# Kernel optimization log

Measured on AMD Instinct MI355X. Metric: run time of the kernel, lower is better.

Reference implementation:

```python
import jax, jax.numpy as jnp
import numpy as np

T, B, H, V = 128, 32, 1024, 32000


def setup_inputs() -> dict:
    key = jax.random.key(0)
    ks = jax.random.split(key, 8)
    scale = 1.0 / np.sqrt(H)
    return {
        "input": jax.random.normal(ks[0], (T, B, H), dtype=jnp.float32),
        "hidden": jnp.zeros((B, H), dtype=jnp.float32),
        "w_ic": jax.random.uniform(ks[1], (H, H), jnp.float32, -scale, scale),
        "w_ix": jax.random.uniform(ks[2], (H, H), jnp.float32, -scale, scale),
        "w_fc": jax.random.uniform(ks[3], (H, H), jnp.float32, -scale, scale),
        "w_fx": jax.random.uniform(ks[4], (H, H), jnp.float32, -scale, scale),
        "b_i": jnp.zeros((H,), dtype=jnp.float32),
        "b_f": jnp.zeros((H,), dtype=jnp.float32),
        "W_out": jax.random.uniform(ks[5], (V, H), jnp.float32, -scale, scale),
        "b_out": jnp.zeros((V,), dtype=jnp.float32),
    }


def reference(input, hidden, w_ic, w_ix, w_fc, w_fx, b_i, b_f, W_out, b_out):
    # Precompute input projections for all timesteps: [T, B, H]
    ix = jnp.einsum("tbh,kh->tbk", input, w_ix)
    fx = jnp.einsum("tbh,kh->tbk", input, w_fx)

    def step(c, xs):
        ix_t, fx_t, x_t = xs
        i_t = jax.nn.sigmoid(c @ w_ic.T + b_i + ix_t)
        f_t = jax.nn.sigmoid(c @ w_fc.T + b_f + fx_t)
        c_new = i_t * x_t + f_t * c  # RAN gated-additive update
        return c_new, c_new

    hidden_final, outputs = jax.lax.scan(step, hidden, (ix, fx, input))
    logits = jnp.einsum("tbh,vh->tbv", outputs, W_out) + b_out
    log_probs = jax.nn.log_softmax(logits, axis=-1)
    return log_probs, hidden_final
```

## Files before the change

### kernel.cpp

```cpp
#include <hip/hip_runtime.h>

typedef __attribute__((ext_vector_type(4))) float f32x4;
typedef __attribute__((ext_vector_type(8))) short bf16x8;

#define T_DIM 128
#define B_DIM 32
#define H_DIM 1024
#define V_DIM 32000
#define MROWS 4096
#define NBLK 64
#define CSTEP 32768
#define WSTRIDE 1028

__device__ __forceinline__ ushort f2bf(float f){
  union { float f; unsigned u; } x; x.f = f;
  unsigned u = x.u;
  unsigned r = (u + 0x7fffu + ((u >> 16) & 1u)) >> 16;
  return (ushort)r;
}
__device__ __forceinline__ float bf2f(ushort h){
  union { unsigned u; float f; } x; x.u = ((unsigned)h) << 16;
  return x.f;
}

__device__ __forceinline__ void async_copy16(void* lds, const void* g){
  __builtin_amdgcn_global_load_lds((const __attribute__((address_space(1))) void*)g,
                                   (__attribute__((address_space(3))) void*)lds, 16, 0, 0);
}

__global__ void cast_bf16_kernel(const float* __restrict__ s, ushort* __restrict__ d, int n4){
  int stride = gridDim.x * blockDim.x;
  for (int i = blockIdx.x*blockDim.x + threadIdx.x; i < n4; i += stride){
    float4 v = ((const float4*)s)[i];
    ushort4 o = make_ushort4(f2bf(v.x), f2bf(v.y), f2bf(v.z), f2bf(v.w));
    ((ushort4*)d)[i] = o;
  }
}

__global__ void cast_split_kernel(const float* __restrict__ s, ushort* __restrict__ dh,
                                  ushort* __restrict__ dl, int n4){
  int stride = gridDim.x * blockDim.x;
  for (int i = blockIdx.x*blockDim.x + threadIdx.x; i < n4; i += stride){
    float4 v = ((const float4*)s)[i];
    ushort4 h = make_ushort4(f2bf(v.x), f2bf(v.y), f2bf(v.z), f2bf(v.w));
    ushort4 l = make_ushort4(f2bf(v.x - bf2f(h.x)), f2bf(v.y - bf2f(h.y)),
                             f2bf(v.z - bf2f(h.z)), f2bf(v.w - bf2f(h.w)));
    ((ushort4*)dh)[i] = h;
    ((ushort4*)dl)[i] = l;
  }
}

__global__ __launch_bounds__(256) void gemm_bt(
    const ushort* __restrict__ A, const ushort* __restrict__ B,
    float* __restrict__ C, const float* __restrict__ bias,
    int N, int K, int NTN, int order, int achunk,
    float* __restrict__ pmax, float* __restrict__ psum)
{
  __shared__ ushort lA[128*32];
  __shared__ ushort lB[128*32];
  __shared__ float pmS[4][64], psS[4][64];
  int tid = threadIdx.x;
  int lane = tid & 63, wid = tid >> 6;
  int bid = blockIdx.x;
  int tm, tn;
  if (order){
    int xcd = bid & 7, id = bid >> 3;
    tn = id >> 2;
    tm = (xcd << 2) | (id & 3);
  } else {
    tm = bid / NTN; tn = bid % NTN;
  }
  int row0 = tm << 7, col0 = tn << 7;

  f32x4 acc[4][4] = {};

  auto stage = [&](const ushort* __restrict__ g, ushort* l, int r0, int k0){
    int c = wid << 1;
    const ushort* s0 = g + (size_t)(r0 + (c<<4) + (lane>>2))*K + k0 + ((lane&3)<<3);
    async_copy16(l + (c<<9), s0);
    async_copy16(l + ((c+1)<<9), s0 + (size_t)16*K);
  };
  auto stageAc = [&](const ushort* __restrict__ g, ushort* l, int r0, int k0){
    int c = wid << 1;
    int cb  = (k0 >> 4) + ((lane & 3) >> 1);
    int sub = (lane & 1) << 3;
    int rA = r0 + (c<<4) + (lane>>2);
    const ushort* sA = g + ((size_t)(rA>>5)<<15) + (cb<<9) + ((rA&31)<<4) + sub;
    async_copy16(l + (c<<9), sA);
    int rB = rA + 16;
    const ushort* sB = g + ((size_t)(rB>>5)<<15) + (cb<<9) + ((rB&31)<<4) + sub;
    async_copy16(l + ((c+1)<<9), sB);
  };

  int nk = K >> 5;
  if (achunk) stageAc(A, lA, row0, 0); else stage(A, lA, row0, 0);
  stage(B, lB, col0, 0);
  int wm = (wid >> 1) << 6, wn = (wid & 1) << 6;
  int kg = (lane >> 4) << 3;
  int ar = lane & 15;

  for (int kt = 0; kt < nk; ++kt){
    __syncthreads();
    bf16x8 af[4], bfr[4];
    #pragma unroll
    for (int mi = 0; mi < 4; ++mi) af[mi]  = *(const bf16x8*)&lA[(wm + mi*16 + ar)*32 + kg];
    #pragma unroll
    for (int ni = 0; ni < 4; ++ni) bfr[ni] = *(const bf16x8*)&lB[(wn + ni*16 + ar)*32 + kg];
    #pragma unroll
    for (int mi = 0; mi < 4; ++mi)
      #pragma unroll
      for (int ni = 0; ni < 4; ++ni)
        acc[mi][ni] = __builtin_amdgcn_mfma_f32_16x16x32_bf16(af[mi], bfr[ni], acc[mi][ni], 0, 0, 0);
    if (kt + 1 < nk){
      __syncthreads();
      if (achunk) stageAc(A, lA, row0, (kt+1) << 5); else stage(A, lA, row0, (kt+1) << 5);
      stage(B, lB, col0, (kt+1) << 5);
    }
  }

  int rr = (lane >> 4) << 2;
  float bb4[4];
  #pragma unroll
  for (int ni = 0; ni < 4; ++ni) bb4[ni] = bias ? bias[col0 + wn + ni*16 + ar] : 0.f;

  #pragma unroll
  for (int mi = 0; mi < 4; ++mi){
    #pragma unroll
    for (int q = 0; q < 4; ++q){
      int r = row0 + wm + mi*16 + rr + q;
      float vals[4];
      #pragma unroll
      for (int ni = 0; ni < 4; ++ni){
        vals[ni] = acc[mi][ni][q] + bb4[ni];
        C[(size_t)r * N + col0 + wn + ni*16 + ar] = vals[ni];
      }
      if (pmax){
        float m = fmaxf(fmaxf(vals[0], vals[1]), fmaxf(vals[2], vals[3]));
        #pragma unroll
        for (int o = 1; o < 16; o <<= 1) m = fmaxf(m, __shfl_xor(m, o));
        float s = expf(vals[0]-m) + expf(vals[1]-m) + expf(vals[2]-m) + expf(vals[3]-m);
        #pragma unroll
        for (int o = 1; o < 16; o <<= 1) s += __shfl_xor(s, o);
        if (ar == 0){ int rl = mi*16 + rr + q; pmS[wid][rl] = m; psS[wid][rl] = s; }
      }
    }
  }
  if (pmax){
    __syncthreads();
    if (tid < 128){
      int rl = tid & 63, half = tid >> 6;
      int w0 = half*2, w1 = w0 + 1;
      float m0 = pmS[w0][rl], m1 = pmS[w1][rl];
      float s0 = psS[w0][rl], s1 = psS[w1][rl];
      float M = fmaxf(m0, m1);
      float S = s0*expf(m0-M) + s1*expf(m1-M);
      int r = row0 + half*64 + rl;
      pmax[(size_t)r*NTN + tn] = M;
      psum[(size_t)r*NTN + tn] = S;
    }
  }
}

__global__ __launch_bounds__(256) void gemm_bt_split(
    const ushort* __restrict__ Ah, const ushort* __restrict__ Al,
    const ushort* __restrict__ Bh, const ushort* __restrict__ Bl,
    float* __restrict__ C, int N, int K, int NTN)
{
  __shared__ ushort lAh[128*32], lAl[128*32], lBh[128*32], lBl[128*32];
  int tid = threadIdx.x;
  int lane = tid & 63, wid = tid >> 6;
  int tm = blockIdx.x / NTN, tn = blockIdx.x % NTN;
  int row0 = tm << 7, col0 = tn << 7;

  f32x4 acc[4][4] = {};

  auto stage = [&](const ushort* __restrict__ g, ushort* l, int r0, int k0){
    int c = wid << 1;
    const ushort* s0 = g + (size_t)(r0 + (c<<4) + (lane>>2))*K + k0 + ((lane&3)<<3);
    async_copy16(l + (c<<9), s0);
    async_copy16(l + ((c+1)<<9), s0 + (size_t)16*K);
  };

  int nk = K >> 5;
  stage(Ah, lAh, row0, 0); stage(Al, lAl, row0, 0);
  stage(Bh, lBh, col0, 0); stage(Bl, lBl, col0, 0);
  int wm = (wid >> 1) << 6, wn = (wid & 1) << 6;
  int kg = (lane >> 4) << 3;
  int ar = lane & 15;

  for (int kt = 0; kt < nk; ++kt){
    __syncthreads();
    bf16x8 afh[4], afl[4], bfh[4], bfl[4];
    #pragma unroll
    for (int mi = 0; mi < 4; ++mi){
      afh[mi] = *(const bf16x8*)&lAh[(wm + mi*16 + ar)*32 + kg];
      afl[mi] = *(const bf16x8*)&lAl[(wm + mi*16 + ar)*32 + kg];
    }
    #pragma unroll
    for (int ni = 0; ni < 4; ++ni){
      bfh[ni] = *(const bf16x8*)&lBh[(wn + ni*16 + ar)*32 + kg];
      bfl[ni] = *(const bf16x8*)&lBl[(wn + ni*16 + ar)*32 + kg];
    }
    #pragma unroll
    for (int mi = 0; mi < 4; ++mi)
      #pragma unroll
      for (int ni = 0; ni < 4; ++ni){
        acc[mi][ni] = __builtin_amdgcn_mfma_f32_16x16x32_bf16(afh[mi], bfh[ni], acc[mi][ni], 0, 0, 0);
        acc[mi][ni] = __builtin_amdgcn_mfma_f32_16x16x32_bf16(afh[mi], bfl[ni], acc[mi][ni], 0, 0, 0);
        acc[mi][ni] = __builtin_amdgcn_mfma_f32_16x16x32_bf16(afl[mi], bfh[ni], acc[mi][ni], 0, 0, 0);
      }
    if (kt + 1 < nk){
      __syncthreads();
      stage(Ah, lAh, row0, (kt+1) << 5); stage(Al, lAl, row0, (kt+1) << 5);
      stage(Bh, lBh, col0, (kt+1) << 5); stage(Bl, lBl, col0, (kt+1) << 5);
    }
  }

  int rr = (lane >> 4) << 2;
  #pragma unroll
  for (int mi = 0; mi < 4; ++mi)
    #pragma unroll
    for (int ni = 0; ni < 4; ++ni){
      int r  = row0 + wm + mi*16 + rr;
      int cc = col0 + wn + ni*16 + ar;
      #pragma unroll
      for (int q = 0; q < 4; ++q)
        C[(size_t)(r + q) * N + cc] = acc[mi][ni][q];
    }
}

__global__ __launch_bounds__(512) void ran_all(
    const ushort* __restrict__ cinit, ushort* __restrict__ cstate,
    const float* __restrict__ hiddenf,
    const ushort* __restrict__ wh, const ushort* __restrict__ wl,
    const float* __restrict__ b_i, const float* __restrict__ b_f,
    const float* __restrict__ ixfx, const float* __restrict__ x_all,
    float* __restrict__ hid_final, unsigned* __restrict__ slots)
{
  __shared__ ushort lWh[32*WSTRIDE];
  __shared__ ushort lWl[32*WSTRIDE];
  __shared__ float part[8][64][4];
  __shared__ float gsm[2*32*17];
  __shared__ float cfl[32][17];

  int tid = threadIdx.x, lane = tid & 63, wid = tid >> 6;
  int kh = wid & 1, mh = (wid >> 1) & 1, gate = wid >> 2;
  int bid = blockIdx.x;
  int nb = bid << 4;
  int ar = lane & 15, kg = (lane >> 4) << 3;
  int um8 = tid >> 3, ukp = (tid & 7) << 1;

  #pragma unroll
  for (int u = 0; u < 8; ++u){
    int unit = u*512 + tid;
    int r = unit >> 7, off = (unit & 127) << 3;
    int g = r >> 4, c = r & 15;
    size_t gsrc = (size_t)((g<<10) + nb + c) * H_DIM + off;
    *(bf16x8*)&lWh[r*WSTRIDE + off] = *(const bf16x8*)&wh[gsrc];
    *(bf16x8*)&lWl[r*WSTRIDE + off] = *(const bf16x8*)&wl[gsrc];
  }
  if (tid < 256){
    cfl[um8][ukp]   = hiddenf[(um8<<10) + nb + ukp];
    cfl[um8][ukp+1] = hiddenf[(um8<<10) + nb + ukp + 1];
  }
  float bb = (gate ? b_f : b_i)[nb + ar];
  const ushort* bbase_h = &lWh[((gate<<4) + ar)*WSTRIDE + (kh<<9)];
  const ushort* bbase_l = &lWl[((gate<<4) + ar)*WSTRIDE + (kh<<9)];
  int abase = (kh<<14) + ((kg>>4)<<9) + (((mh<<4) + ar)<<4) + (kg & 8);
  __syncthreads();

  float2 xv2; float pix[4];
  if (tid < 256) xv2 = *(const float2*)&x_all[(um8<<10) + nb + ukp];
  if (kh == 0){
    #pragma unroll
    for (int q = 0; q < 4; ++q){
      int m = (mh<<4) + ((lane>>4)<<2) + q;
      pix[q] = ixfx[m*2048 + (gate<<10) + nb + ar];
    }
  }

  for (int t = 0; t < T_DIM; ++t){
    const ushort* cst = t ? cstate + (size_t)(t-1)*CSTEP : cinit;

    f32x4 a0 = {}, a1 = {};
    #pragma unroll 4
    for (int kk = 0; kk < 16; ++kk){
      int oa = abase + (kk<<10);
      int ob = (kk<<5) + kg;
      bf16x8 vah = *(const bf16x8*)&cst[oa];
      bf16x8 vbh = *(const bf16x8*)&bbase_h[ob];
      bf16x8 vbl = *(const bf16x8*)&bbase_l[ob];
      a0 = __builtin_amdgcn_mfma_f32_16x16x32_bf16(vah, vbh, a0, 0, 0, 0);
      a1 = __builtin_amdgcn_mfma_f32_16x16x32_bf16(vah, vbl, a1, 0, 0, 0);
    }
    f32x4 acc = a0 + a1;
    *(f32x4*)&part[wid][lane][0] = acc;
    __syncthreads();
    if (kh == 0){
      f32x4 sum = *(const f32x4*)&part[wid][lane][0] + *(const f32x4*)&part[wid+1][lane][0];
      #pragma unroll
      for (int q = 0; q < 4; ++q){
        int m = (mh<<4) + ((lane>>4)<<2) + q;
        float pre = sum[q] + bb + pix[q];
        gsm[((gate<<5) + m)*17 + ar] = 1.f / (1.f + expf(-pre));
      }
    }
    __syncthreads();
    if (tid < 256){
      float iv0 = gsm[um8*17 + ukp],       iv1 = gsm[um8*17 + ukp + 1];
      float fv0 = gsm[(32+um8)*17 + ukp],  fv1 = gsm[(32+um8)*17 + ukp + 1];
      float c0 = cfl[um8][ukp], c1 = cfl[um8][ukp+1];
      float n0 = iv0*xv2.x + fv0*c0;
      float n1 = iv1*xv2.y + fv1*c1;
      cfl[um8][ukp] = n0; cfl[um8][ukp+1] = n1;
      unsigned hp = (unsigned)f2bf(n0) | ((unsigned)f2bf(n1) << 16);
      size_t cb = (size_t)t*CSTEP + (bid<<9) + (um8<<4) + ukp;
      __hip_atomic_store((unsigned*)&cstate[cb], hp, __ATOMIC_RELAXED, __HIP_MEMORY_SCOPE_AGENT);
      if (t == T_DIM-1){
        int rb = (um8<<10) + nb + ukp;
        hid_final[rb] = n0; hid_final[rb+1] = n1;
      }
    }
    if (t < T_DIM-1){
      __syncthreads();
      if (tid == 0)
        __hip_atomic_store(&slots[bid], (unsigned)(t+1), __ATOMIC_RELAXED, __HIP_MEMORY_SCOPE_AGENT);
      {
        const float* x_t  = x_all + (size_t)(t+1)*(B_DIM*H_DIM);
        const float* ix_t = ixfx  + (size_t)(t+1)*(B_DIM*2048);
        if (tid < 256) xv2 = *(const float2*)&x_t[(um8<<10) + nb + ukp];
        if (kh == 0){
          #pragma unroll
          for (int q = 0; q < 4; ++q){
            int m = (mh<<4) + ((lane>>4)<<2) + q;
            pix[q] = ix_t[m*2048 + (gate<<10) + nb + ar];
          }
        }
      }
      if (wid == 0){
        unsigned tgt = (unsigned)(t+1);
        while (1){
          unsigned v = __hip_atomic_load(&slots[lane], __ATOMIC_RELAXED, __HIP_MEMORY_SCOPE_AGENT);
          if (__ballot(v < tgt) == 0ull) break;
          __builtin_amdgcn_s_sleep(1);
        }
      }
      __syncthreads();
    }
  }
}

__global__ void init_c_kernel(const float* __restrict__ hidden,
                              ushort* __restrict__ cinit, unsigned* __restrict__ slots){
  int i = blockIdx.x * blockDim.x + threadIdx.x;
  if (blockIdx.x == 0 && threadIdx.x < NBLK) slots[threadIdx.x] = 0;
  float v = hidden[i];
  int m = i >> 10, col = i & 1023;
  cinit[((col>>4)<<9) + (m<<4) + (col&15)] = f2bf(v);
}

__global__ __launch_bounds__(64) void lse_reduce(const float* __restrict__ pmax,
                                                 const float* __restrict__ psum,
                                                 float* __restrict__ lse, int ntn){
  int row = blockIdx.x, lane = threadIdx.x;
  float m = -1e30f, s = 0.f;
  for (int i = lane; i < ntn; i += 64){
    float mi = pmax[(size_t)row*ntn + i], si = psum[(size_t)row*ntn + i];
    float M = fmaxf(m, mi);
    s = s*expf(m - M) + si*expf(mi - M);
    m = M;
  }
  #pragma unroll
  for (int o = 32; o; o >>= 1){
    float m2 = __shfl_xor(m, o), s2 = __shfl_xor(s, o);
    float M = fmaxf(m, m2);
    s = s*expf(m - M) + s2*expf(m2 - M);
    m = M;
  }
  if (lane == 0) lse[row] = m + logf(s);
}

__global__ __launch_bounds__(256) void sub_kernel(float* __restrict__ logits,
                                                  const float* __restrict__ lse){
  size_t row = blockIdx.x;
  float l = lse[row];
  float4* p4 = (float4*)(logits + row * (size_t)V_DIM);
  for (int i = threadIdx.x; i < V_DIM/4; i += 256){
    float4 v = p4[i];
    v.x -= l; v.y -= l; v.z -= l; v.w -= l;
    p4[i] = v;
  }
}

extern "C" void kernel_launch(void* const* d_in, const int* in_sizes, int n_in,
                              void* d_out, int out_size, void* d_ws, size_t ws_size,
                              hipStream_t stream)
{
  const float* input  = (const float*)d_in[0];
  const float* hidden = (const float*)d_in[1];
  const float* w_ic   = (const float*)d_in[2];
  const float* w_ix   = (const float*)d_in[3];
  const float* w_fc   = (const float*)d_in[4];
  const float* w_fx   = (const float*)d_in[5];
  const float* b_i    = (const float*)d_in[6];
  const float* b_f    = (const float*)d_in[7];
  const float* W_out  = (const float*)d_in[8];
  const float* b_out  = (const float*)d_in[9];
  float* out = (float*)d_out;

  char* ws = (char*)d_ws;
  ushort* wout_bf = (ushort*)(ws + 0);
  ushort* in_hi   = (ushort*)(ws + 65536000);
  ushort* in_lo   = (ushort*)(ws + 73924608);
  ushort* wx_hi   = (ushort*)(ws + 82313216);
  ushort* wx_lo   = (ushort*)(ws + 86507520);
  ushort* wc_hi   = (ushort*)(ws + 90701824);
  ushort* wc_lo   = (ushort*)(ws + 94896128);
  unsigned* slots = (unsigned*)(ws + 107479040);
  ushort* cinit   = (ushort*)(ws + 107479296);
  ushort* cstate  = in_hi;
  float*  pmax    = (float*)in_lo;
  float*  psum    = (float*)(ws + 78020608);
  float*  lse     = (float*)wx_hi;
  float*  ixfx    = out;

  cast_bf16_kernel <<<2048,256,0,stream>>>(W_out, wout_bf, V_DIM*H_DIM/4);
  cast_split_kernel<<<1024,256,0,stream>>>(input, in_hi, in_lo, MROWS*H_DIM/4);
  cast_split_kernel<<<256,256,0,stream>>>(w_ix, wx_hi,             wx_lo,             H_DIM*H_DIM/4);
  cast_split_kernel<<<256,256,0,stream>>>(w_fx, wx_hi+H_DIM*H_DIM, wx_lo+H_DIM*H_DIM, H_DIM*H_DIM/4);
  cast_split_kernel<<<256,256,0,stream>>>(w_ic, wc_hi,             wc_lo,             H_DIM*H_DIM/4);
  cast_split_kernel<<<256,256,0,stream>>>(w_fc, wc_hi+H_DIM*H_DIM, wc_lo+H_DIM*H_DIM, H_DIM*H_DIM/4);

  gemm_bt_split<<<32*16,256,0,stream>>>(in_hi, in_lo, wx_hi, wx_lo, ixfx, 2048, H_DIM, 16);

  init_c_kernel<<<128,256,0,stream>>>(hidden, cinit, slots);

  ran_all<<<NBLK,512,0,stream>>>(cinit, cstate, hidden, wc_hi, wc_lo, b_i, b_f,
                                 ixfx, input, out + (size_t)MROWS*V_DIM, slots);

  gemm_bt<<<32*250,256,0,stream>>>(cstate, wout_bf, out, b_out, V_DIM, H_DIM, 250, 1, 1, pmax, psum);
  lse_reduce<<<MROWS,64,0,stream>>>(pmax, psum, lse, 250);
  sub_kernel<<<MROWS,256,0,stream>>>(out, lse);
}
```

Measured before the change: 2.045 ms.

## Split recurrent matvec K four ways and share A loads across both gates

Each wave in the persistent recurrent kernel now covers a quarter of K for one batch half and computes both gates, so each state (A) fragment loaded from global memory feeds four MFMAs instead of two. All eight A loads are issued up front before the MFMA chain to hide global latency. The partial sums are then reduced four ways through shared memory, and the barrier spin-wait moves to wave 7. This cuts redundant global reads of the state on the serial per-timestep critical path, at the cost of more registers and a wider reduction.

```diff
diff --git a/kernel.cpp b/kernel.cpp
--- a/kernel.cpp
+++ b/kernel.cpp
@@ -239,12 +239,13 @@
 {
   __shared__ ushort lWh[32*WSTRIDE];
   __shared__ ushort lWl[32*WSTRIDE];
-  __shared__ float part[8][64][4];
+  __shared__ f32x4 part[4][2][2][64];
   __shared__ float gsm[2*32*17];
   __shared__ float cfl[32][17];
 
   int tid = threadIdx.x, lane = tid & 63, wid = tid >> 6;
-  int kh = wid & 1, mh = (wid >> 1) & 1, gate = wid >> 2;
+  int kq = wid & 3, mh = wid >> 2;
+  int rgate = wid & 1, rmh = wid >> 1;
   int bid = blockIdx.x;
   int nb = bid << 4;
   int ar = lane & 15, kg = (lane >> 4) << 3;
@@ -263,49 +264,61 @@
     cfl[um8][ukp]   = hiddenf[(um8<<10) + nb + ukp];
     cfl[um8][ukp+1] = hiddenf[(um8<<10) + nb + ukp + 1];
   }
-  float bb = (gate ? b_f : b_i)[nb + ar];
-  const ushort* bbase_h = &lWh[((gate<<4) + ar)*WSTRIDE + (kh<<9)];
-  const ushort* bbase_l = &lWl[((gate<<4) + ar)*WSTRIDE + (kh<<9)];
-  int abase = (kh<<14) + ((kg>>4)<<9) + (((mh<<4) + ar)<<4) + (kg & 8);
+  float bb = (rgate ? b_f : b_i)[nb + ar];
+  const ushort* b0h = &lWh[(     ar)*WSTRIDE + (kq<<8) + kg];
+  const ushort* b0l = &lWl[(     ar)*WSTRIDE + (kq<<8) + kg];
+  const ushort* b1h = &lWh[(16 + ar)*WSTRIDE + (kq<<8) + kg];
+  const ushort* b1l = &lWl[(16 + ar)*WSTRIDE + (kq<<8) + kg];
+  int abase = (kq<<13) + ((kg>>4)<<9) + (((mh<<4) + ar)<<4) + (kg & 8);
   __syncthreads();
 
   float2 xv2; float pix[4];
   if (tid < 256) xv2 = *(const float2*)&x_all[(um8<<10) + nb + ukp];
-  if (kh == 0){
+  if (wid < 4){
     #pragma unroll
     for (int q = 0; q < 4; ++q){
-      int m = (mh<<4) + ((lane>>4)<<2) + q;
-      pix[q] = ixfx[m*2048 + (gate<<10) + nb + ar];
+      int m = (rmh<<4) + ((lane>>4)<<2) + q;
+      pix[q] = ixfx[m*2048 + (rgate<<10) + nb + ar];
     }
   }
 
   for (int t = 0; t < T_DIM; ++t){
     const ushort* cst = t ? cstate + (size_t)(t-1)*CSTEP : cinit;
 
-    f32x4 a0 = {}, a1 = {};
-    #pragma unroll 4
-    for (int kk = 0; kk < 16; ++kk){
-      int oa = abase + (kk<<10);
-      int ob = (kk<<5) + kg;
-      bf16x8 vah = *(const bf16x8*)&cst[oa];
-      bf16x8 vbh = *(const bf16x8*)&bbase_h[ob];
-      bf16x8 vbl = *(const bf16x8*)&bbase_l[ob];
-      a0 = __builtin_amdgcn_mfma_f32_16x16x32_bf16(vah, vbh, a0, 0, 0, 0);
-      a1 = __builtin_amdgcn_mfma_f32_16x16x32_bf16(vah, vbl, a1, 0, 0, 0);
-    }
-    f32x4 acc = a0 + a1;
-    *(f32x4*)&part[wid][lane][0] = acc;
+    bf16x8 a[8];
+    #pragma unroll
+    for (int kk = 0; kk < 8; ++kk)
+      a[kk] = *(const bf16x8*)&cst[abase + (kk<<10)];
+
+    f32x4 g0h = {}, g0l = {}, g1h = {}, g1l = {};
+    #pragma unroll
+    for (int kk = 0; kk < 8; ++kk){
+      int ob = kk << 5;
+      bf16x8 w0h = *(const bf16x8*)&b0h[ob];
+      bf16x8 w0l = *(const bf16x8*)&b0l[ob];
+      bf16x8 w1h = *(const bf16x8*)&b1h[ob];
+      bf16x8 w1l = *(const bf16x8*)&b1l[ob];
+      g0h = __builtin_amdgcn_mfma_f32_16x16x32_bf16(a[kk], w0h, g0h, 0, 0, 0);
+      g0l = __builtin_amdgcn_mfma_f32_16x16x32_bf16(a[kk], w0l, g0l, 0, 0, 0);
+      g1h = __builtin_amdgcn_mfma_f32_16x16x32_bf16(a[kk], w1h, g1h, 0, 0, 0);
+      g1l = __builtin_amdgcn_mfma_f32_16x16x32_bf16(a[kk], w1l, g1l, 0, 0, 0);
+    }
+    part[kq][mh][0][lane] = g0h + g0l;
+    part[kq][mh][1][lane] = g1h + g1l;
     __syncthreads();
-    if (kh == 0){
-      f32x4 sum = *(const f32x4*)&part[wid][lane][0] + *(const f32x4*)&part[wid+1][lane][0];
+
+    if (wid < 4){
+      f32x4 sum = part[0][rmh][rgate][lane] + part[1][rmh][rgate][lane]
+                + part[2][rmh][rgate][lane] + part[3][rmh][rgate][lane];
       #pragma unroll
       for (int q = 0; q < 4; ++q){
-        int m = (mh<<4) + ((lane>>4)<<2) + q;
+        int m = (rmh<<4) + ((lane>>4)<<2) + q;
         float pre = sum[q] + bb + pix[q];
-        gsm[((gate<<5) + m)*17 + ar] = 1.f / (1.f + expf(-pre));
+        gsm[((rgate<<5) + m)*17 + ar] = 1.f / (1.f + expf(-pre));
       }
     }
     __syncthreads();
+
     if (tid < 256){
       float iv0 = gsm[um8*17 + ukp],       iv1 = gsm[um8*17 + ukp + 1];
       float fv0 = gsm[(32+um8)*17 + ukp],  fv1 = gsm[(32+um8)*17 + ukp + 1];
@@ -329,15 +342,15 @@
         const float* x_t  = x_all + (size_t)(t+1)*(B_DIM*H_DIM);
         const float* ix_t = ixfx  + (size_t)(t+1)*(B_DIM*2048);
         if (tid < 256) xv2 = *(const float2*)&x_t[(um8<<10) + nb + ukp];
-        if (kh == 0){
+        if (wid < 4){
           #pragma unroll
           for (int q = 0; q < 4; ++q){
-            int m = (mh<<4) + ((lane>>4)<<2) + q;
-            pix[q] = ix_t[m*2048 + (gate<<10) + nb + ar];
+            int m = (rmh<<4) + ((lane>>4)<<2) + q;
+            pix[q] = ix_t[m*2048 + (rgate<<10) + nb + ar];
           }
         }
       }
-      if (wid == 0){
+      if (wid == 7){
         unsigned tgt = (unsigned)(t+1);
         while (1){
           unsigned v = __hip_atomic_load(&slots[lane], __ATOMIC_RELAXED, __HIP_MEMORY_SCOPE_AGENT);
```

Measured after the change: 2.037 ms. About the same (-0.4%).
